# Kernel optimization log

Hardware: AMD Instinct MI355X
Metric: run time of the kernel (lower is better)

## Reference

```python
import jax, jax.numpy as jnp
import numpy as np

B_AGENTS = 262144
N = 17  # 9 needs (0:9) + 4 actions (9:13) + 4 valences (13:17)

# Fixed Grossberg constants (registered buffers in the torch module)
TAU, DECAY, B_CAP, C_FLOOR = 0.8, 0.15, 1.0, 0.1
LAT_INHIB, DIV_SIGMA = 3.0, 0.3
ALPHA, BETA = 1.5, 0.75


def setup_inputs() -> dict:
    key = jax.random.key(0)
    ks = jax.random.split(key, 6)
    return {
        "t": jax.random.normal(ks[0], (1,), jnp.float32),
        "state": jax.random.uniform(ks[1], (B_AGENTS, N), jnp.float32),
        "W_pos": jax.random.uniform(ks[2], (B_AGENTS, N, N), jnp.float32),
        "W_neg": jax.random.uniform(ks[3], (B_AGENTS, N, N), jnp.float32),
        "feasibility": jax.random.uniform(ks[4], (B_AGENTS, 4), jnp.float32),
        "perturbation": jax.random.normal(ks[5], (B_AGENTS, N), jnp.float32),
    }


def _grossberg(state, W_pos, W_neg, feasibility, perturbation):
    bs = state.shape[0]
    dt = state.dtype
    ones9 = jnp.ones((bs, 9), dt)
    ones4 = jnp.ones((bs, 4), dt)
    zeros8 = jnp.zeros((bs, 8), dt)   # action+valence columns (9:17)
    zeros9 = jnp.zeros((bs, 9), dt)

    valences = state[:, 13:17]
    valences_eval = valences + perturbation[:, 13:17]
    P_needs = perturbation[:, 0:9]
    E_env_needs = jax.nn.relu(P_needs)
    I_env_needs = jax.nn.relu(-P_needs)

    # gates are 1 everywhere except the 4 action rows
    gate_exc = jnp.concatenate([ones9, jax.nn.sigmoid(ALPHA * valences_eval), ones4], axis=1)
    gate_inh = jnp.concatenate([ones9, jax.nn.sigmoid(-BETA * valences_eval), ones4], axis=1)

    # gated tiny bmm per agent: (gate_i * W_ij) @ state_j, fused into one einsum
    excitation = jnp.einsum('bi,bij,bj->bi', gate_exc, W_pos, state)
    inhibition_W = jnp.einsum('bi,bij,bj->bi', gate_inh, W_neg, state)

    E_env_full = jnp.concatenate([E_env_needs, zeros8], axis=1)
    I_env_full = jnp.concatenate([I_env_needs, zeros8], axis=1)
    total_excitation = excitation + E_env_full

    # selective lateral inhibition among the 4 actions
    actions = state[:, 9:13]
    other_action = jnp.sum(actions, axis=1, keepdims=True) - actions
    lateral = LAT_INHIB * other_action / (DIV_SIGMA + other_action + 1e-6)
    lateral_full = jnp.concatenate([zeros9, lateral, jnp.zeros((bs, 4), dt)], axis=1)

    total_inhibition = inhibition_W + lateral_full + I_env_full

    dS_dt = (-DECAY * state
             + (B_CAP - state) * jax.nn.relu(total_excitation)
             - (C_FLOOR + state) * jax.nn.relu(total_inhibition)) / TAU

    mask = jnp.concatenate([ones9, feasibility, ones4], axis=1)
    return dS_dt * mask


def reference(t, state, W_pos, W_neg, feasibility, perturbation):
    # t is unused by the dynamics (autonomous ODE), kept for signature fidelity
    return _grossberg(state, W_pos, W_neg, feasibility, perturbation)
```

## Files before the change

### kernel.cpp

```cpp
#include <hip/hip_runtime.h>

#define B_AGENTS 262144
#define NN 17
#define BLOCK 256
#define CHUNK (BLOCK * NN)
#define CHUNK4 (CHUNK / 4)

__global__ __launch_bounds__(BLOCK) void grossberg_kernel(
    const float* __restrict__ state,
    const float* __restrict__ W_pos,
    const float* __restrict__ W_neg,
    const float* __restrict__ feas,
    const float* __restrict__ pert,
    float* __restrict__ out)
{
    __shared__ float lwp[CHUNK];
    __shared__ float lwn[CHUNK];

    const int tid = threadIdx.x;
    const size_t base = (size_t)blockIdx.x * CHUNK;

    const float4* __restrict__ gp = (const float4*)(W_pos + base);
    const float4* __restrict__ gn = (const float4*)(W_neg + base);
    float4* lp = (float4*)lwp;
    float4* ln = (float4*)lwn;
    #pragma unroll
    for (int it = 0; it < 4; ++it) {
        const int k = tid + it * BLOCK;
        lp[k] = gp[k];
        ln[k] = gn[k];
    }
    if (tid < CHUNK4 - 4 * BLOCK) {
        const int k = tid + 4 * BLOCK;
        lp[k] = gp[k];
        ln[k] = gn[k];
    }

    const int t = blockIdx.x * BLOCK + tid;
    const int b = t / NN;
    const int i = t - b * NN;

    float sv[NN];
    const float* __restrict__ s = state + b * NN;
    #pragma unroll
    for (int j = 0; j < NN; ++j) sv[j] = s[j];

    __syncthreads();

    const float* wpr = lwp + tid * NN;
    const float* wnr = lwn + tid * NN;
    float sum_p = 0.f, sum_n = 0.f;
    #pragma unroll
    for (int j = 0; j < NN; ++j) {
        sum_p = fmaf(wpr[j], sv[j], sum_p);
        sum_n = fmaf(wnr[j], sv[j], sum_n);
    }

    float gate_e = 1.f, gate_i = 1.f;
    float env_e = 0.f, env_i = 0.f;
    float lat = 0.f, mask = 1.f;

    if (i < 9) {
        const float p = pert[b * NN + i];
        env_e = fmaxf(p, 0.f);
        env_i = fmaxf(-p, 0.f);
    } else if (i < 13) {
        const float v = sv[i + 4] + pert[b * NN + i + 4];
        gate_e = 1.f / (1.f + __expf(-1.5f * v));
        gate_i = 1.f / (1.f + __expf(0.75f * v));
        const float sum_act = sv[9] + sv[10] + sv[11] + sv[12];
        const float other = sum_act - sv[i];
        lat = 3.0f * other / (0.3f + other + 1e-6f);
        mask = feas[b * 4 + (i - 9)];
    }

    const float te = gate_e * sum_p + env_e;
    const float ti = gate_i * sum_n + lat + env_i;
    const float si = sv[i];

    const float dS = (-0.15f * si
                      + (1.0f - si) * fmaxf(te, 0.f)
                      - (0.1f + si) * fmaxf(ti, 0.f)) * 1.25f;

    out[t] = dS * mask;
}

extern "C" void kernel_launch(void* const* d_in, const int* in_sizes, int n_in,
                              void* d_out, int out_size, void* d_ws, size_t ws_size,
                              hipStream_t stream)
{
    const float* state = (const float*)d_in[1];
    const float* W_pos = (const float*)d_in[2];
    const float* W_neg = (const float*)d_in[3];
    const float* feas  = (const float*)d_in[4];
    const float* pert  = (const float*)d_in[5];
    float* out = (float*)d_out;

    const int total = B_AGENTS * NN;
    const int grid = total / BLOCK;
    grossberg_kernel<<<grid, BLOCK, 0, stream>>>(state, W_pos, W_neg, feas, pert, out);
}
```

Measured before the change: 118.5 us.

## Persistent grid with register prefetch of next weight chunk

Replaces the one-block-per-chunk launch with a fixed grid of 2176 persistent blocks that stride over chunks. Each block loads the next chunk's W_pos/W_neg tiles into registers while computing on the current chunk in shared memory, overlapping global loads with compute. This costs extra registers (40 floats for the prefetch buffers) and an additional barrier per iteration, which may lower occupancy on a bandwidth-bound kernel.

Result: slower. 283.0 us (+138.9%).

```diff
diff --git a/kernel.cpp b/kernel.cpp
--- a/kernel.cpp
+++ b/kernel.cpp
@@ -3,8 +3,10 @@
 #define B_AGENTS 262144
 #define NN 17
 #define BLOCK 256
-#define CHUNK (BLOCK * NN)
-#define CHUNK4 (CHUNK / 4)
+#define CHUNK_FLOATS (BLOCK * NN)
+#define CHUNK4 (CHUNK_FLOATS / 4)
+#define NCHUNKS (B_AGENTS * NN / BLOCK)
+#define GRID 2176
 
 __global__ __launch_bounds__(BLOCK) void grossberg_kernel(
     const float* __restrict__ state,
@@ -14,75 +16,88 @@
     const float* __restrict__ pert,
     float* __restrict__ out)
 {
-    __shared__ float lwp[CHUNK];
-    __shared__ float lwn[CHUNK];
+    __shared__ float lwp[CHUNK_FLOATS];
+    __shared__ float lwn[CHUNK_FLOATS];
 
     const int tid = threadIdx.x;
-    const size_t base = (size_t)blockIdx.x * CHUNK;
+    const bool tail = (tid < CHUNK4 - 4 * BLOCK);
 
-    const float4* __restrict__ gp = (const float4*)(W_pos + base);
-    const float4* __restrict__ gn = (const float4*)(W_neg + base);
-    float4* lp = (float4*)lwp;
-    float4* ln = (float4*)lwn;
-    #pragma unroll
-    for (int it = 0; it < 4; ++it) {
-        const int k = tid + it * BLOCK;
-        lp[k] = gp[k];
-        ln[k] = gn[k];
-    }
-    if (tid < CHUNK4 - 4 * BLOCK) {
-        const int k = tid + 4 * BLOCK;
-        lp[k] = gp[k];
-        ln[k] = gn[k];
+    float4 rp[5], rn[5];
+    int c = blockIdx.x;
+    {
+        const float4* __restrict__ gp = (const float4*)W_pos + (size_t)c * CHUNK4;
+        const float4* __restrict__ gn = (const float4*)W_neg + (size_t)c * CHUNK4;
+        #pragma unroll
+        for (int it = 0; it < 4; ++it) { rp[it] = gp[tid + it * BLOCK]; rn[it] = gn[tid + it * BLOCK]; }
+        if (tail) { rp[4] = gp[tid + 4 * BLOCK]; rn[4] = gn[tid + 4 * BLOCK]; }
     }
 
-    const int t = blockIdx.x * BLOCK + tid;
-    const int b = t / NN;
-    const int i = t - b * NN;
+    for (; c < NCHUNKS; c += GRID) {
+        const int t = c * BLOCK + tid;
+        const int b = t / NN;
+        const int i = t - b * NN;
 
-    float sv[NN];
-    const float* __restrict__ s = state + b * NN;
-    #pragma unroll
-    for (int j = 0; j < NN; ++j) sv[j] = s[j];
+        float sv[NN];
+        const float* __restrict__ s = state + b * NN;
+        #pragma unroll
+        for (int j = 0; j < NN; ++j) sv[j] = s[j];
 
-    __syncthreads();
+        __syncthreads();
 
-    const float* wpr = lwp + tid * NN;
-    const float* wnr = lwn + tid * NN;
-    float sum_p = 0.f, sum_n = 0.f;
-    #pragma unroll
-    for (int j = 0; j < NN; ++j) {
-        sum_p = fmaf(wpr[j], sv[j], sum_p);
-        sum_n = fmaf(wnr[j], sv[j], sum_n);
+        float4* lp = (float4*)lwp;
+        float4* ln = (float4*)lwn;
+        #pragma unroll
+        for (int it = 0; it < 4; ++it) { lp[tid + it * BLOCK] = rp[it]; ln[tid + it * BLOCK] = rn[it]; }
+        if (tail) { lp[tid + 4 * BLOCK] = rp[4]; ln[tid + 4 * BLOCK] = rn[4]; }
+
+        __syncthreads();
+
+        const int cn = c + GRID;
+        if (cn < NCHUNKS) {
+            const float4* __restrict__ gp = (const float4*)W_pos + (size_t)cn * CHUNK4;
+            const float4* __restrict__ gn = (const float4*)W_neg + (size_t)cn * CHUNK4;
+            #pragma unroll
+            for (int it = 0; it < 4; ++it) { rp[it] = gp[tid + it * BLOCK]; rn[it] = gn[tid + it * BLOCK]; }
+            if (tail) { rp[4] = gp[tid + 4 * BLOCK]; rn[4] = gn[tid + 4 * BLOCK]; }
+        }
+
+        const float* wpr = lwp + tid * NN;
+        const float* wnr = lwn + tid * NN;
+        float sum_p = 0.f, sum_n = 0.f;
+        #pragma unroll
+        for (int j = 0; j < NN; ++j) {
+            sum_p = fmaf(wpr[j], sv[j], sum_p);
+            sum_n = fmaf(wnr[j], sv[j], sum_n);
+        }
+
+        float gate_e = 1.f, gate_i = 1.f;
+        float env_e = 0.f, env_i = 0.f;
+        float lat = 0.f, mask = 1.f;
+
+        if (i < 9) {
+            const float p = pert[b * NN + i];
+            env_e = fmaxf(p, 0.f);
+            env_i = fmaxf(-p, 0.f);
+        } else if (i < 13) {
+            const float v = sv[i + 4] + pert[b * NN + i + 4];
+            gate_e = 1.f / (1.f + __expf(-1.5f * v));
+            gate_i = 1.f / (1.f + __expf(0.75f * v));
+            const float sum_act = sv[9] + sv[10] + sv[11] + sv[12];
+            const float other = sum_act - sv[i];
+            lat = 3.0f * other / (0.3f + other + 1e-6f);
+            mask = feas[b * 4 + (i - 9)];
+        }
+
+        const float te = gate_e * sum_p + env_e;
+        const float ti = gate_i * sum_n + lat + env_i;
+        const float si = sv[i];
+
+        const float dS = (-0.15f * si
+                          + (1.0f - si) * fmaxf(te, 0.f)
+                          - (0.1f + si) * fmaxf(ti, 0.f)) * 1.25f;
+
+        out[t] = dS * mask;
     }
-
-    float gate_e = 1.f, gate_i = 1.f;
-    float env_e = 0.f, env_i = 0.f;
-    float lat = 0.f, mask = 1.f;
-
-    if (i < 9) {
-        const float p = pert[b * NN + i];
-        env_e = fmaxf(p, 0.f);
-        env_i = fmaxf(-p, 0.f);
-    } else if (i < 13) {
-        const float v = sv[i + 4] + pert[b * NN + i + 4];
-        gate_e = 1.f / (1.f + __expf(-1.5f * v));
-        gate_i = 1.f / (1.f + __expf(0.75f * v));
-        const float sum_act = sv[9] + sv[10] + sv[11] + sv[12];
-        const float other = sum_act - sv[i];
-        lat = 3.0f * other / (0.3f + other + 1e-6f);
-        mask = feas[b * 4 + (i - 9)];
-    }
-
-    const float te = gate_e * sum_p + env_e;
-    const float ti = gate_i * sum_n + lat + env_i;
-    const float si = sv[i];
-
-    const float dS = (-0.15f * si
-                      + (1.0f - si) * fmaxf(te, 0.f)
-                      - (0.1f + si) * fmaxf(ti, 0.f)) * 1.25f;
-
-    out[t] = dS * mask;
 }
 
 extern "C" void kernel_launch(void* const* d_in, const int* in_sizes, int n_in,
@@ -96,7 +111,5 @@
     const float* pert  = (const float*)d_in[5];
     float* out = (float*)d_out;
 
-    const int total = B_AGENTS * NN;
-    const int grid = total / BLOCK;
-    grossberg_kernel<<<grid, BLOCK, 0, stream>>>(state, W_pos, W_neg, feas, pert, out);
+    grossberg_kernel<<<GRID, BLOCK, 0, stream>>>(state, W_pos, W_neg, feas, pert, out);
 }
```
